# Kernel optimization log

Hardware: AMD Instinct MI355X
Metric: run time of the kernel (lower is better)

Reference implementation:

```python
import jax, jax.numpy as jnp
import numpy as np
import math

HEAD_DIM = 128
DEPTH = 12
LAMBDA_INIT = 0.8 - 0.6 * math.exp(-0.3 * DEPTH)
EPS = 1e-5


def setup_inputs() -> dict:
    key = jax.random.key(0)
    ks = jax.random.split(key, 7)
    B, S, H2, D = 2, 2048, 16, HEAD_DIM  # H2 = 2 * num_diff_heads
    q = jax.random.normal(ks[0], (B, S, H2, D), dtype=jnp.float32)
    k = jax.random.normal(ks[1], (B, S, H2, D), dtype=jnp.float32)
    v = jax.random.normal(ks[2], (B, S, H2, D), dtype=jnp.float32)
    lambda_q1 = 0.1 * jax.random.normal(ks[3], (D,), dtype=jnp.float32)
    lambda_k1 = 0.1 * jax.random.normal(ks[4], (D,), dtype=jnp.float32)
    lambda_q2 = 0.1 * jax.random.normal(ks[5], (D,), dtype=jnp.float32)
    lambda_k2 = 0.1 * jax.random.normal(ks[6], (D,), dtype=jnp.float32)
    return {"q": q, "k": k, "v": v, "lambda_q1": lambda_q1, "lambda_k1": lambda_k1,
            "lambda_q2": lambda_q2, "lambda_k2": lambda_k2}


def _attn(qh, kh, v12, scale, causal_bias):
    # qh,kh: [B,S,H,D]; v12: [B,S,H,2D] (concat of v1,v2 -> same softmax shared,
    # identical math to the two separate flash calls attnX1/attnX2 concatenated)
    scores = jnp.einsum('bshd,bthd->bhst', qh, kh) * scale + causal_bias
    p = jax.nn.softmax(scores, axis=-1)
    return jnp.einsum('bhst,bthd->bshd', p, v12)  # [B,S,H,2D]


def reference(q, k, v, lambda_q1, lambda_k1, lambda_q2, lambda_k2):
    B, S, H2, D = q.shape
    H = H2 // 2
    scale = 1.0 / math.sqrt(D)
    # split_heads: '(H two) D' -> pairs of adjacent heads
    def split(x):
        x = x.reshape(B, S, H, 2, D)
        return x[..., 0, :], x[..., 1, :]
    q1, q2 = split(q)
    k1, k2 = split(k)
    v1, v2 = split(v)
    v12 = jnp.concatenate([v1, v2], axis=-1)  # [B,S,H,2D]

    causal_bias = jnp.where(jnp.tril(jnp.ones((S, S), dtype=bool)), 0.0,
                            jnp.float32(-jnp.inf))  # [S,S]

    attn1 = _attn(q1, k1, v12, scale, causal_bias)  # = cat(attn11, attn12)
    attn2 = _attn(q2, k2, v12, scale, causal_bias)  # = cat(attn21, attn22)

    lambda_1 = jnp.exp(jnp.sum(lambda_q1 * lambda_k1))
    lambda_2 = jnp.exp(jnp.sum(lambda_q2 * lambda_k2))
    lambda_full = lambda_1 - lambda_2 + LAMBDA_INIT

    attn = attn1 - lambda_full * attn2  # [B,S,H,2D]
    # RMSNorm over last dim (2D), no affine
    attn = attn * jax.lax.rsqrt(jnp.mean(attn * attn, axis=-1, keepdims=True) + EPS)
    attn = attn * (1.0 - LAMBDA_INIT)
    # '... H (two D) -> ... (H two) D'
    return attn.reshape(B, S, H, 2, D).reshape(B, S, H2, D)
```

## Files before the change

kernel.cpp:

```cpp
#include <hip/hip_runtime.h>
#include <math.h>


#define S_LEN 2048
#define ROWSTR 2048
#define NEG_BIG (-3.0e38f)
#define QSCALE (1.44269504088896f * 0.0883883476483184f)
#define SM_SHIFT 20.0f
#define LAMBDA_INIT 0.783605766532f

typedef __attribute__((ext_vector_type(8))) short short8;
typedef __attribute__((ext_vector_type(4))) float f32x4;

__device__ __forceinline__ short f2bf(float f) {
    unsigned u = __builtin_bit_cast(unsigned, f);
    u += 0x7fffu + ((u >> 16) & 1u);
    return (short)(u >> 16);
}

__device__ __forceinline__ void async16(const short* g, short* l) {
    __builtin_amdgcn_global_load_lds(
        (const __attribute__((address_space(1))) unsigned int*)g,
        (__attribute__((address_space(3))) unsigned int*)l, 16, 0, 0);
}

__global__ __launch_bounds__(256)
void prep_kernel(const float* __restrict__ k, const float* __restrict__ v,
                 short* __restrict__ kws, short* __restrict__ vws) {
    __shared__ short sT[32][258];
    const int tid = threadIdx.x;
    const int bh  = blockIdx.x >> 6;
    const int t   = blockIdx.x & 63;
    const int b   = bh >> 3;
    const int h   = bh & 7;

    {
        const int attn = tid >> 7;
        const int key  = (tid >> 2) & 31;
        const int tt   = tid & 3;
        const int s    = t * 32 + key;
        const float* src = k + (((size_t)(b * S_LEN + s) * 16) + 2 * h + attn) * 128 + tt * 32;
        short* kdst = kws + (((size_t)(bh * 64 + t)) << 13) + attn * 4096 + key * 128;
        #pragma unroll
        for (int i = 0; i < 4; ++i) {
            const int c = tt * 4 + i;
            float4 a0 = *(const float4*)(src + i * 8);
            float4 a1 = *(const float4*)(src + i * 8 + 4);
            short8 sv;
            sv[0]=f2bf(a0.x); sv[1]=f2bf(a0.y); sv[2]=f2bf(a0.z); sv[3]=f2bf(a0.w);
            sv[4]=f2bf(a1.x); sv[5]=f2bf(a1.y); sv[6]=f2bf(a1.z); sv[7]=f2bf(a1.w);
            *(short8*)(kdst + ((c ^ (key & 7)) << 3)) = sv;
        }
    }

    {
        const int key  = tid >> 3;
        const int part = tid & 7;
        const float* vsrc = v + (((size_t)(b * S_LEN + t * 32 + key) * 16) + 2 * h) * 128 + part * 32;
        #pragma unroll
        for (int i = 0; i < 4; ++i) {
            float4 a0 = *(const float4*)(vsrc + i * 8);
            float4 a1 = *(const float4*)(vsrc + i * 8 + 4);
            short8 sv;
            sv[0]=f2bf(a0.x); sv[1]=f2bf(a0.y); sv[2]=f2bf(a0.z); sv[3]=f2bf(a0.w);
            sv[4]=f2bf(a1.x); sv[5]=f2bf(a1.y); sv[6]=f2bf(a1.z); sv[7]=f2bf(a1.w);
            *(short8*)(&sT[key][part * 32 + i * 8]) = sv;
        }
    }
    __syncthreads();

    {
        short vv[32];
        #pragma unroll
        for (int key = 0; key < 32; ++key)
            vv[key] = sT[key][tid];
        short* vdst = vws + (((size_t)(bh * 64 + t)) << 13) + tid * 32;
        #pragma unroll
        for (int i = 0; i < 4; ++i)
            *(short8*)(vdst + i * 8) = *(short8*)&vv[i * 8];
    }
}

__global__ __launch_bounds__(256, 2)
void fda_kernel(const float* __restrict__ q,
                const short* __restrict__ kws, const short* __restrict__ vws,
                const float* __restrict__ lq1, const float* __restrict__ lk1,
                const float* __restrict__ lq2, const float* __restrict__ lk2,
                float* __restrict__ out) {
    __shared__ short sK[2][2][32][128];
    __shared__ short sV[2][256][32];
    __shared__ short sP[2][64][40];
    __shared__ float sL[2][64];
    __shared__ float sRed[2][2][32];

    const int tid  = threadIdx.x;
    const int w    = tid >> 6;
    const int lane = tid & 63;
    const int mi   = lane & 15;
    const int quad = lane >> 4;
    const int rg   = w & 1;
    const int u    = w >> 1;

    const int bid = blockIdx.x;
    const int bh  = bid & 15;
    const int g   = bid >> 4;
    const int qt  = (g < 16) ? (31 - g) : (g - 16);
    const int b   = bh >> 3;
    const int h   = bh & 7;
    const int qbase = qt * 64;
    const int nt  = 2 * qt + 2;

    const short* ktile0 = kws + (((size_t)(bh * 64)) << 13);
    const short* vtile0 = vws + (((size_t)(bh * 64)) << 13);

    {
        short* dk = &sK[0][0][0][0];
        short* dv = &sV[0][0][0];
        #pragma unroll
        for (int i = 0; i < 4; ++i) {
            const int ch = (w * 4 + i) * 512;
            async16(ktile0 + ch + lane * 8, dk + ch);
            async16(vtile0 + ch + lane * 8, dv + ch);
        }
    }

    float d1 = lq1[lane] * lk1[lane] + lq1[lane + 64] * lk1[lane + 64];
    float d2 = lq2[lane] * lk2[lane] + lq2[lane + 64] * lk2[lane + 64];
    #pragma unroll
    for (int off = 32; off; off >>= 1) {
        d1 += __shfl_xor(d1, off);
        d2 += __shfl_xor(d2, off);
    }
    const float lambda_full = expf(d1) - expf(d2) + LAMBDA_INIT;

    short8 qf[2][4];
    {
        #pragma unroll
        for (int m = 0; m < 2; ++m) {
            const int row = qbase + rg * 32 + m * 16 + mi;
            const float* qr = q + (((size_t)(b * S_LEN + row) * 16) + 2 * h + u) * 128 + quad * 8;
            #pragma unroll
            for (int db = 0; db < 4; ++db) {
                float4 a0 = *(const float4*)(qr + db * 32);
                float4 a1 = *(const float4*)(qr + db * 32 + 4);
                short8 sv;
                sv[0]=f2bf(a0.x*QSCALE); sv[1]=f2bf(a0.y*QSCALE); sv[2]=f2bf(a0.z*QSCALE); sv[3]=f2bf(a0.w*QSCALE);
                sv[4]=f2bf(a1.x*QSCALE); sv[5]=f2bf(a1.y*QSCALE); sv[6]=f2bf(a1.z*QSCALE); sv[7]=f2bf(a1.w*QSCALE);
                qf[m][db] = sv;
            }
        }
    }

    float l[2][4] = {{0.f,0.f,0.f,0.f},{0.f,0.f,0.f,0.f}};
    f32x4 O[2][2][8];
    #pragma unroll
    for (int a = 0; a < 2; ++a)
        #pragma unroll
        for (int m = 0; m < 2; ++m)
            #pragma unroll
            for (int nb = 0; nb < 8; ++nb)
                O[a][m][nb] = (f32x4){0.f, 0.f, 0.f, 0.f};

    for (int t = 0; t < nt; ++t) {
        __syncthreads();
        const int buf = t & 1;
        const bool act = (t <= 2 * qt + rg);

        if (act) {
            f32x4 S[2][2];
            #pragma unroll
            for (int m = 0; m < 2; ++m)
                #pragma unroll
                for (int kh = 0; kh < 2; ++kh)
                    S[m][kh] = (f32x4){0.f, 0.f, 0.f, 0.f};
            const short* kb = &sK[buf][u][0][0];
            #pragma unroll
            for (int db = 0; db < 4; ++db) {
                #pragma unroll
                for (int kh = 0; kh < 2; ++kh) {
                    const short8 kf = *(const short8*)(kb + (kh * 16 + mi) * 128 +
                                       ((((db << 2) + quad) ^ (mi & 7)) << 3));
                    S[0][kh] = __builtin_amdgcn_mfma_f32_16x16x32_bf16(qf[0][db], kf, S[0][kh], 0, 0, 0);
                    S[1][kh] = __builtin_amdgcn_mfma_f32_16x16x32_bf16(qf[1][db], kf, S[1][kh], 0, 0, 0);
                }
            }
            if (t == 2 * qt + rg) {
                const int qr0 = qbase + rg * 32;
                #pragma unroll
                for (int m = 0; m < 2; ++m)
                    #pragma unroll
                    for (int kh = 0; kh < 2; ++kh)
                        #pragma unroll
                        for (int r = 0; r < 4; ++r)
                            if (t * 32 + kh * 16 + mi > qr0 + m * 16 + quad * 4 + r)
                                S[m][kh][r] = NEG_BIG;
            }
            #pragma unroll
            for (int m = 0; m < 2; ++m) {
                short* pp = &sP[u][rg * 32 + m * 16 + quad * 4][mi];
                #pragma unroll
                for (int r = 0; r < 4; ++r) {
                    const float pa = exp2f(S[m][0][r] - SM_SHIFT);
                    const float pb = exp2f(S[m][1][r] - SM_SHIFT);
                    l[m][r] += pa + pb;
                    pp[r * 40]      = f2bf(pa);
                    pp[r * 40 + 16] = f2bf(pb);
                }
            }
        }
        __syncthreads();

        if (t + 1 < nt) {
            const short* kt = ktile0 + (((size_t)(t + 1)) << 13);
            const short* vt = vtile0 + (((size_t)(t + 1)) << 13);
            short* dk = &sK[buf ^ 1][0][0][0];
            short* dv = &sV[buf ^ 1][0][0];
            #pragma unroll
            for (int i = 0; i < 4; ++i) {
                const int ch = (w * 4 + i) * 512;
                async16(kt + ch + lane * 8, dk + ch);
                async16(vt + ch + lane * 8, dv + ch);
            }
        }

        if (act) {
            short8 pA[2][2];
            #pragma unroll
            for (int a = 0; a < 2; ++a)
                #pragma unroll
                for (int m = 0; m < 2; ++m)
                    pA[a][m] = *(const short8*)&sP[a][rg * 32 + m * 16 + mi][quad * 8];
            #pragma unroll
            for (int nb = 0; nb < 8; ++nb) {
                const short8 bv = *(const short8*)&sV[buf][u * 128 + nb * 16 + mi][quad * 8];
                O[0][0][nb] = __builtin_amdgcn_mfma_f32_16x16x32_bf16(pA[0][0], bv, O[0][0][nb], 0, 0, 0);
                O[0][1][nb] = __builtin_amdgcn_mfma_f32_16x16x32_bf16(pA[0][1], bv, O[0][1][nb], 0, 0, 0);
                O[1][0][nb] = __builtin_amdgcn_mfma_f32_16x16x32_bf16(pA[1][0], bv, O[1][0][nb], 0, 0, 0);
                O[1][1][nb] = __builtin_amdgcn_mfma_f32_16x16x32_bf16(pA[1][1], bv, O[1][1][nb], 0, 0, 0);
            }
        }
    }

    #pragma unroll
    for (int m = 0; m < 2; ++m)
        #pragma unroll
        for (int r = 0; r < 4; ++r) {
            float s = l[m][r];
            s += __shfl_xor(s, 1); s += __shfl_xor(s, 2);
            s += __shfl_xor(s, 4); s += __shfl_xor(s, 8);
            l[m][r] = s;
        }
    if (mi == 0) {
        #pragma unroll
        for (int m = 0; m < 2; ++m)
            #pragma unroll
            for (int r = 0; r < 4; ++r)
                sL[u][rg * 32 + m * 16 + quad * 4 + r] = l[m][r];
    }
    __syncthreads();

    float ss[2][4] = {{0.f,0.f,0.f,0.f},{0.f,0.f,0.f,0.f}};
    #pragma unroll
    for (int m = 0; m < 2; ++m)
        #pragma unroll
        for (int r = 0; r < 4; ++r) {
            const int row = rg * 32 + m * 16 + quad * 4 + r;
            const float il1 = 1.0f / sL[0][row];
            const float il2 = lambda_full / sL[1][row];
            #pragma unroll
            for (int nb = 0; nb < 8; ++nb) {
                const float c = O[0][m][nb][r] * il1 - O[1][m][nb][r] * il2;
                O[0][m][nb][r] = c;
                ss[m][r] += c * c;
            }
        }
    #pragma unroll
    for (int m = 0; m < 2; ++m)
        #pragma unroll
        for (int r = 0; r < 4; ++r) {
            float s = ss[m][r];
            s += __shfl_xor(s, 1); s += __shfl_xor(s, 2);
            s += __shfl_xor(s, 4); s += __shfl_xor(s, 8);
            ss[m][r] = s;
        }
    if (mi == 0) {
        #pragma unroll
        for (int m = 0; m < 2; ++m)
            #pragma unroll
            for (int r = 0; r < 4; ++r)
                sRed[rg][u][m * 16 + quad * 4 + r] = ss[m][r];
    }
    __syncthreads();

    #pragma unroll
    for (int m = 0; m < 2; ++m)
        #pragma unroll
        for (int r = 0; r < 4; ++r) {
            const int rl  = m * 16 + quad * 4 + r;
            const float tot = ss[m][r] + sRed[rg][u ^ 1][rl];
            const float scale = rsqrtf(tot * (1.0f / 256.0f) + 1e-5f) * (1.0f - LAMBDA_INIT);
            const int gr = qbase + rg * 32 + rl;
            float* ob = out + ((size_t)(b * S_LEN + gr)) * ROWSTR + h * 256 + u * 128 + mi;
            #pragma unroll
            for (int nb = 0; nb < 8; ++nb)
                ob[nb * 16] = O[0][m][nb][r] * scale;
        }
}

extern "C" void kernel_launch(void* const* d_in, const int* in_sizes, int n_in,
                              void* d_out, int out_size, void* d_ws, size_t ws_size,
                              hipStream_t stream) {
    (void)in_sizes; (void)n_in; (void)out_size; (void)ws_size;
    const float* q   = (const float*)d_in[0];
    const float* k   = (const float*)d_in[1];
    const float* v   = (const float*)d_in[2];
    const float* lq1 = (const float*)d_in[3];
    const float* lk1 = (const float*)d_in[4];
    const float* lq2 = (const float*)d_in[5];
    const float* lk2 = (const float*)d_in[6];
    float* out = (float*)d_out;

    short* kws = (short*)d_ws;
    short* vws = kws + (size_t)16 * 64 * 8192;

    prep_kernel<<<dim3(1024), dim3(256), 0, stream>>>(k, v, kws, vws);
    fda_kernel<<<dim3(512), dim3(256), 0, stream>>>(q, kws, vws,
                                                    lq1, lk1, lq2, lk2, out);
}
```

Before: 252.7 us.

## Keep softmax probabilities in registers via transposed S and redistribute PV work

Computes S transposed (K as the A operand) so the exp'd probabilities land directly in the MFMA B-operand layout, which removes the sP shared-memory round trip and one barrier per tile. Each wave now accumulates its own attention's P against the full 256-wide V. The two attention outputs are then combined through a shared-memory exchange in the epilogue. The prep kernel stages K through LDS for coalesced stores and permutes V keys to match the new P layout, and the next-tile prefetch is issued earlier in the loop. The cost is twice the O accumulator registers per wave and an extra LDS exchange at the end, which may hurt occupancy.

```diff
diff --git a/kernel.cpp b/kernel.cpp
--- a/kernel.cpp
+++ b/kernel.cpp
@@ -27,7 +27,8 @@
 __global__ __launch_bounds__(256)
 void prep_kernel(const float* __restrict__ k, const float* __restrict__ v,
                  short* __restrict__ kws, short* __restrict__ vws) {
-    __shared__ short sT[32][258];
+    __shared__ short sKL[8192];
+    __shared__ short sT[32][260];
     const int tid = threadIdx.x;
     const int bh  = blockIdx.x >> 6;
     const int t   = blockIdx.x & 63;
@@ -35,45 +36,57 @@
     const int h   = bh & 7;
 
     {
-        const int attn = tid >> 7;
-        const int key  = (tid >> 2) & 31;
-        const int tt   = tid & 3;
-        const int s    = t * 32 + key;
-        const float* src = k + (((size_t)(b * S_LEN + s) * 16) + 2 * h + attn) * 128 + tt * 32;
-        short* kdst = kws + (((size_t)(bh * 64 + t)) << 13) + attn * 4096 + key * 128;
+        const int lh    = tid & 31;
+        const int c     = lh >> 1;
+        const int half  = lh & 1;
+        const int rbase = tid >> 5;
+        #pragma unroll
+        for (int p = 0; p < 8; ++p) {
+            const int row  = p * 8 + rbase;
+            const int attn = row >> 5;
+            const int key  = row & 31;
+            const float* src = k + (((size_t)(b * S_LEN + t * 32 + key) * 16) + 2 * h + attn) * 128 + lh * 4;
+            const float4 a = *(const float4*)src;
+            short4 sv;
+            sv.x = f2bf(a.x); sv.y = f2bf(a.y); sv.z = f2bf(a.z); sv.w = f2bf(a.w);
+            *(short4*)(sKL + attn * 4096 + key * 128 + ((c ^ (key & 7)) << 3) + half * 4) = sv;
+        }
+    }
+
+    {
+        const int n0 = (tid & 63) * 4;
+        const int kb = tid >> 6;
+        #pragma unroll
+        for (int p = 0; p < 8; ++p) {
+            const int key = p * 4 + kb;
+            const float* src = v + (((size_t)(b * S_LEN + t * 32 + key) * 16) + 2 * h) * 128 + n0;
+            const float4 a = *(const float4*)src;
+            short4 sv;
+            sv.x = f2bf(a.x); sv.y = f2bf(a.y); sv.z = f2bf(a.z); sv.w = f2bf(a.w);
+            *(short4*)(&sT[key][n0]) = sv;
+        }
+    }
+    __syncthreads();
+
+    {
+        short* kdst = kws + (((size_t)(bh * 64 + t)) << 13);
         #pragma unroll
         for (int i = 0; i < 4; ++i) {
-            const int c = tt * 4 + i;
-            float4 a0 = *(const float4*)(src + i * 8);
-            float4 a1 = *(const float4*)(src + i * 8 + 4);
-            short8 sv;
-            sv[0]=f2bf(a0.x); sv[1]=f2bf(a0.y); sv[2]=f2bf(a0.z); sv[3]=f2bf(a0.w);
-            sv[4]=f2bf(a1.x); sv[5]=f2bf(a1.y); sv[6]=f2bf(a1.z); sv[7]=f2bf(a1.w);
-            *(short8*)(kdst + ((c ^ (key & 7)) << 3)) = sv;
-        }
-    }
-
-    {
-        const int key  = tid >> 3;
-        const int part = tid & 7;
-        const float* vsrc = v + (((size_t)(b * S_LEN + t * 32 + key) * 16) + 2 * h) * 128 + part * 32;
-        #pragma unroll
-        for (int i = 0; i < 4; ++i) {
-            float4 a0 = *(const float4*)(vsrc + i * 8);
-            float4 a1 = *(const float4*)(vsrc + i * 8 + 4);
-            short8 sv;
-            sv[0]=f2bf(a0.x); sv[1]=f2bf(a0.y); sv[2]=f2bf(a0.z); sv[3]=f2bf(a0.w);
-            sv[4]=f2bf(a1.x); sv[5]=f2bf(a1.y); sv[6]=f2bf(a1.z); sv[7]=f2bf(a1.w);
-            *(short8*)(&sT[key][part * 32 + i * 8]) = sv;
-        }
-    }
-    __syncthreads();
-
-    {
+            const short8 d = *(const short8*)(sKL + i * 2048 + tid * 8);
+            *(short8*)(kdst + i * 2048 + tid * 8) = d;
+        }
+    }
+
+    {
+        const int f = (tid >> 1) & 3;
         short vv[32];
         #pragma unroll
-        for (int key = 0; key < 32; ++key)
-            vv[key] = sT[key][tid];
+        for (int o = 0; o < 32; ++o) {
+            const int kh = (o >> 2) & 1;
+            const int s  = o & 3;
+            const int C  = o >> 3;
+            vv[o] = sT[kh * 16 + ((C ^ f) << 2) + s][tid];
+        }
         short* vdst = vws + (((size_t)(bh * 64 + t)) << 13) + tid * 32;
         #pragma unroll
         for (int i = 0; i < 4; ++i)
@@ -87,11 +100,12 @@
                 const float* __restrict__ lq1, const float* __restrict__ lk1,
                 const float* __restrict__ lq2, const float* __restrict__ lk2,
                 float* __restrict__ out) {
-    __shared__ short sK[2][2][32][128];
-    __shared__ short sV[2][256][32];
-    __shared__ short sP[2][64][40];
-    __shared__ float sL[2][64];
-    __shared__ float sRed[2][2][32];
+    __shared__ __align__(16) char smemRaw[66560];
+    short* sK   = (short*)smemRaw;
+    short* sV   = (short*)(smemRaw + 32768);
+    float* sL   = (float*)(smemRaw + 65536);
+    float* sRed = (float*)(smemRaw + 66048);
+    float* xbuf = (float*)smemRaw;
 
     const int tid  = threadIdx.x;
     const int w    = tid >> 6;
@@ -114,13 +128,11 @@
     const short* vtile0 = vws + (((size_t)(bh * 64)) << 13);
 
     {
-        short* dk = &sK[0][0][0][0];
-        short* dv = &sV[0][0][0];
         #pragma unroll
         for (int i = 0; i < 4; ++i) {
             const int ch = (w * 4 + i) * 512;
-            async16(ktile0 + ch + lane * 8, dk + ch);
-            async16(vtile0 + ch + lane * 8, dv + ch);
+            async16(ktile0 + ch + lane * 8, sK + ch);
+            async16(vtile0 + ch + lane * 8, sV + ch);
         }
     }
 
@@ -134,146 +146,152 @@
     const float lambda_full = expf(d1) - expf(d2) + LAMBDA_INIT;
 
     short8 qf[2][4];
-    {
-        #pragma unroll
-        for (int m = 0; m < 2; ++m) {
-            const int row = qbase + rg * 32 + m * 16 + mi;
-            const float* qr = q + (((size_t)(b * S_LEN + row) * 16) + 2 * h + u) * 128 + quad * 8;
-            #pragma unroll
-            for (int db = 0; db < 4; ++db) {
-                float4 a0 = *(const float4*)(qr + db * 32);
-                float4 a1 = *(const float4*)(qr + db * 32 + 4);
-                short8 sv;
-                sv[0]=f2bf(a0.x*QSCALE); sv[1]=f2bf(a0.y*QSCALE); sv[2]=f2bf(a0.z*QSCALE); sv[3]=f2bf(a0.w*QSCALE);
-                sv[4]=f2bf(a1.x*QSCALE); sv[5]=f2bf(a1.y*QSCALE); sv[6]=f2bf(a1.z*QSCALE); sv[7]=f2bf(a1.w*QSCALE);
-                qf[m][db] = sv;
-            }
-        }
-    }
-
-    float l[2][4] = {{0.f,0.f,0.f,0.f},{0.f,0.f,0.f,0.f}};
-    f32x4 O[2][2][8];
-    #pragma unroll
-    for (int a = 0; a < 2; ++a)
-        #pragma unroll
-        for (int m = 0; m < 2; ++m)
-            #pragma unroll
-            for (int nb = 0; nb < 8; ++nb)
-                O[a][m][nb] = (f32x4){0.f, 0.f, 0.f, 0.f};
+    #pragma unroll
+    for (int m = 0; m < 2; ++m) {
+        const int row = qbase + rg * 32 + m * 16 + mi;
+        const float* qr = q + (((size_t)(b * S_LEN + row) * 16) + 2 * h + u) * 128 + quad * 8;
+        #pragma unroll
+        for (int db = 0; db < 4; ++db) {
+            float4 a0 = *(const float4*)(qr + db * 32);
+            float4 a1 = *(const float4*)(qr + db * 32 + 4);
+            short8 sv;
+            sv[0]=f2bf(a0.x*QSCALE); sv[1]=f2bf(a0.y*QSCALE); sv[2]=f2bf(a0.z*QSCALE); sv[3]=f2bf(a0.w*QSCALE);
+            sv[4]=f2bf(a1.x*QSCALE); sv[5]=f2bf(a1.y*QSCALE); sv[6]=f2bf(a1.z*QSCALE); sv[7]=f2bf(a1.w*QSCALE);
+            qf[m][db] = sv;
+        }
+    }
+
+    float l[2] = {0.f, 0.f};
+    f32x4 O[2][16];
+    #pragma unroll
+    for (int m = 0; m < 2; ++m)
+        #pragma unroll
+        for (int nb = 0; nb < 16; ++nb)
+            O[m][nb] = (f32x4){0.f, 0.f, 0.f, 0.f};
+
+    const int vswz = (quad ^ ((mi >> 1) & 3)) << 3;
 
     for (int t = 0; t < nt; ++t) {
         __syncthreads();
         const int buf = t & 1;
+
+        if (t + 1 < nt) {
+            const short* kt = ktile0 + (((size_t)(t + 1)) << 13);
+            const short* vt = vtile0 + (((size_t)(t + 1)) << 13);
+            short* dk = sK + (buf ^ 1) * 8192;
+            short* dv = sV + (buf ^ 1) * 8192;
+            #pragma unroll
+            for (int i = 0; i < 4; ++i) {
+                const int ch = (w * 4 + i) * 512;
+                async16(kt + ch + lane * 8, dk + ch);
+                async16(vt + ch + lane * 8, dv + ch);
+            }
+        }
+
         const bool act = (t <= 2 * qt + rg);
-
         if (act) {
-            f32x4 S[2][2];
+            f32x4 ST[2][2];
             #pragma unroll
             for (int m = 0; m < 2; ++m)
                 #pragma unroll
                 for (int kh = 0; kh < 2; ++kh)
-                    S[m][kh] = (f32x4){0.f, 0.f, 0.f, 0.f};
-            const short* kb = &sK[buf][u][0][0];
+                    ST[m][kh] = (f32x4){0.f, 0.f, 0.f, 0.f};
+            const short* kb = sK + buf * 8192 + u * 4096;
             #pragma unroll
             for (int db = 0; db < 4; ++db) {
                 #pragma unroll
                 for (int kh = 0; kh < 2; ++kh) {
                     const short8 kf = *(const short8*)(kb + (kh * 16 + mi) * 128 +
                                        ((((db << 2) + quad) ^ (mi & 7)) << 3));
-                    S[0][kh] = __builtin_amdgcn_mfma_f32_16x16x32_bf16(qf[0][db], kf, S[0][kh], 0, 0, 0);
-                    S[1][kh] = __builtin_amdgcn_mfma_f32_16x16x32_bf16(qf[1][db], kf, S[1][kh], 0, 0, 0);
+                    ST[0][kh] = __builtin_amdgcn_mfma_f32_16x16x32_bf16(kf, qf[0][db], ST[0][kh], 0, 0, 0);
+                    ST[1][kh] = __builtin_amdgcn_mfma_f32_16x16x32_bf16(kf, qf[1][db], ST[1][kh], 0, 0, 0);
                 }
             }
             if (t == 2 * qt + rg) {
-                const int qr0 = qbase + rg * 32;
-                #pragma unroll
-                for (int m = 0; m < 2; ++m)
+                #pragma unroll
+                for (int m = 0; m < 2; ++m) {
+                    const int qrow = qbase + rg * 32 + m * 16 + mi;
                     #pragma unroll
                     for (int kh = 0; kh < 2; ++kh)
                         #pragma unroll
                         for (int r = 0; r < 4; ++r)
-                            if (t * 32 + kh * 16 + mi > qr0 + m * 16 + quad * 4 + r)
-                                S[m][kh][r] = NEG_BIG;
-            }
+                            if (t * 32 + kh * 16 + quad * 4 + r > qrow)
+                                ST[m][kh][r] = NEG_BIG;
+                }
+            }
+            short8 pB[2];
             #pragma unroll
             for (int m = 0; m < 2; ++m) {
-                short* pp = &sP[u][rg * 32 + m * 16 + quad * 4][mi];
-                #pragma unroll
-                for (int r = 0; r < 4; ++r) {
-                    const float pa = exp2f(S[m][0][r] - SM_SHIFT);
-                    const float pb = exp2f(S[m][1][r] - SM_SHIFT);
-                    l[m][r] += pa + pb;
-                    pp[r * 40]      = f2bf(pa);
-                    pp[r * 40 + 16] = f2bf(pb);
-                }
-            }
-        }
-        __syncthreads();
-
-        if (t + 1 < nt) {
-            const short* kt = ktile0 + (((size_t)(t + 1)) << 13);
-            const short* vt = vtile0 + (((size_t)(t + 1)) << 13);
-            short* dk = &sK[buf ^ 1][0][0][0];
-            short* dv = &sV[buf ^ 1][0][0];
-            #pragma unroll
-            for (int i = 0; i < 4; ++i) {
-                const int ch = (w * 4 + i) * 512;
-                async16(kt + ch + lane * 8, dk + ch);
-                async16(vt + ch + lane * 8, dv + ch);
-            }
-        }
-
-        if (act) {
-            short8 pA[2][2];
-            #pragma unroll
-            for (int a = 0; a < 2; ++a)
-                #pragma unroll
-                for (int m = 0; m < 2; ++m)
-                    pA[a][m] = *(const short8*)&sP[a][rg * 32 + m * 16 + mi][quad * 8];
-            #pragma unroll
-            for (int nb = 0; nb < 8; ++nb) {
-                const short8 bv = *(const short8*)&sV[buf][u * 128 + nb * 16 + mi][quad * 8];
-                O[0][0][nb] = __builtin_amdgcn_mfma_f32_16x16x32_bf16(pA[0][0], bv, O[0][0][nb], 0, 0, 0);
-                O[0][1][nb] = __builtin_amdgcn_mfma_f32_16x16x32_bf16(pA[0][1], bv, O[0][1][nb], 0, 0, 0);
-                O[1][0][nb] = __builtin_amdgcn_mfma_f32_16x16x32_bf16(pA[1][0], bv, O[1][0][nb], 0, 0, 0);
-                O[1][1][nb] = __builtin_amdgcn_mfma_f32_16x16x32_bf16(pA[1][1], bv, O[1][1][nb], 0, 0, 0);
-            }
-        }
-    }
-
-    #pragma unroll
-    for (int m = 0; m < 2; ++m)
-        #pragma unroll
-        for (int r = 0; r < 4; ++r) {
-            float s = l[m][r];
-            s += __shfl_xor(s, 1); s += __shfl_xor(s, 2);
-            s += __shfl_xor(s, 4); s += __shfl_xor(s, 8);
-            l[m][r] = s;
-        }
-    if (mi == 0) {
-        #pragma unroll
-        for (int m = 0; m < 2; ++m)
-            #pragma unroll
-            for (int r = 0; r < 4; ++r)
-                sL[u][rg * 32 + m * 16 + quad * 4 + r] = l[m][r];
+                #pragma unroll
+                for (int kh = 0; kh < 2; ++kh)
+                    #pragma unroll
+                    for (int r = 0; r < 4; ++r) {
+                        const float p = exp2f(ST[m][kh][r] - SM_SHIFT);
+                        l[m] += p;
+                        pB[m][kh * 4 + r] = f2bf(p);
+                    }
+            }
+            const short* vb = sV + buf * 8192;
+            #pragma unroll
+            for (int nb = 0; nb < 16; ++nb) {
+                const short8 bv = *(const short8*)(vb + (nb * 16 + mi) * 32 + vswz);
+                O[0][nb] = __builtin_amdgcn_mfma_f32_16x16x32_bf16(pB[0], bv, O[0][nb], 0, 0, 0);
+                O[1][nb] = __builtin_amdgcn_mfma_f32_16x16x32_bf16(pB[1], bv, O[1][nb], 0, 0, 0);
+            }
+        }
+    }
+
+    #pragma unroll
+    for (int m = 0; m < 2; ++m) {
+        float lm = l[m];
+        lm += __shfl_xor(lm, 16);
+        lm += __shfl_xor(lm, 32);
+        if (quad == 0) sL[u * 64 + rg * 32 + m * 16 + mi] = lm;
     }
     __syncthreads();
 
-    float ss[2][4] = {{0.f,0.f,0.f,0.f},{0.f,0.f,0.f,0.f}};
     #pragma unroll
     for (int m = 0; m < 2; ++m)
         #pragma unroll
         for (int r = 0; r < 4; ++r) {
             const int row = rg * 32 + m * 16 + quad * 4 + r;
-            const float il1 = 1.0f / sL[0][row];
-            const float il2 = lambda_full / sL[1][row];
-            #pragma unroll
-            for (int nb = 0; nb < 8; ++nb) {
-                const float c = O[0][m][nb][r] * il1 - O[1][m][nb][r] * il2;
-                O[0][m][nb][r] = c;
-                ss[m][r] += c * c;
-            }
-        }
+            const float fac = (u == 0) ? (1.0f / sL[row])
+                                       : (lambda_full / sL[64 + row]);
+            #pragma unroll
+            for (int nb = 0; nb < 16; ++nb)
+                O[m][nb][r] *= fac;
+        }
+    {
+        const int base = (rg * 2 + u) << 12;
+        #pragma unroll
+        for (int m = 0; m < 2; ++m)
+            #pragma unroll
+            for (int nbs = 0; nbs < 8; ++nbs) {
+                const int nb = (1 - u) * 8 + nbs;
+                #pragma unroll
+                for (int r = 0; r < 4; ++r)
+                    xbuf[base + (m * 16 + quad * 4 + r) * 128 + nbs * 16 + mi] = O[m][nb][r];
+            }
+    }
+    __syncthreads();
+
+    float ss[2][4] = {{0.f,0.f,0.f,0.f},{0.f,0.f,0.f,0.f}};
+    {
+        const int rbase = (rg * 2 + (u ^ 1)) << 12;
+        #pragma unroll
+        for (int m = 0; m < 2; ++m)
+            #pragma unroll
+            for (int nbs = 0; nbs < 8; ++nbs) {
+                const int nb = u * 8 + nbs;
+                #pragma unroll
+                for (int r = 0; r < 4; ++r) {
+                    const float rv = xbuf[rbase + (m * 16 + quad * 4 + r) * 128 + nbs * 16 + mi];
+                    const float c = (u == 0) ? (O[m][nb][r] - rv) : (rv - O[m][nb][r]);
+                    O[m][nb][r] = c;
+                    ss[m][r] += c * c;
+                }
+            }
+    }
     #pragma unroll
     for (int m = 0; m < 2; ++m)
         #pragma unroll
@@ -288,7 +306,7 @@
         for (int m = 0; m < 2; ++m)
             #pragma unroll
             for (int r = 0; r < 4; ++r)
-                sRed[rg][u][m * 16 + quad * 4 + r] = ss[m][r];
+                sRed[((rg * 2 + u) << 5) + m * 16 + quad * 4 + r] = ss[m][r];
     }
     __syncthreads();
 
@@ -297,13 +315,15 @@
         #pragma unroll
         for (int r = 0; r < 4; ++r) {
             const int rl  = m * 16 + quad * 4 + r;
-            const float tot = ss[m][r] + sRed[rg][u ^ 1][rl];
+            const float tot = ss[m][r] + sRed[((rg * 2 + (u ^ 1)) << 5) + rl];
             const float scale = rsqrtf(tot * (1.0f / 256.0f) + 1e-5f) * (1.0f - LAMBDA_INIT);
             const int gr = qbase + rg * 32 + rl;
-            float* ob = out + ((size_t)(b * S_LEN + gr)) * ROWSTR + h * 256 + u * 128 + mi;
-            #pragma unroll
-            for (int nb = 0; nb < 8; ++nb)
-                ob[nb * 16] = O[0][m][nb][r] * scale;
+            float* ob = out + ((size_t)(b * S_LEN + gr)) * ROWSTR + h * 256 + mi;
+            #pragma unroll
+            for (int nbs = 0; nbs < 8; ++nbs) {
+                const int nb = u * 8 + nbs;
+                ob[nb * 16] = O[m][nb][r] * scale;
+            }
         }
 }
 
```

Measured after the change: 888.9 us. 252% more time.
